# Optimization experiments

Measured on AMD Instinct MI355X. Metric: run time of the kernel, lower is better.

Reference implementation:

```python
import jax, jax.numpy as jnp
import numpy as np
from jax import lax

B, N, NC = 16, 25200, 80
CONF_THRES = 0.25
IOU_THRES = 0.45
TOP_K = 1024      # pre-NMS candidates (fixed for jit)
MAX_DET = 300     # max detections kept per image (YOLOv5 default)
MAX_WH = 4096.0   # per-class box offset trick (class-aware NMS)
IMG = 640.0


def setup_inputs() -> dict:
    key = jax.random.key(0)
    k1, k2 = jax.random.split(key)
    raw = jax.random.uniform(k1, (B, N, 5 + NC), dtype=jnp.float32)
    # xywh boxes in pixel coords, obj/cls scores in [0,1]
    xy = raw[..., :2] * IMG
    wh = raw[..., 2:4] * 128.0 + 4.0
    scores = raw[..., 4:]
    detections = jnp.concatenate([xy, wh, scores], axis=-1)
    return {"detections": detections}


def _xywh2xyxy(b):
    xy, wh = b[..., :2], b[..., 2:4]
    half = wh * 0.5
    return jnp.concatenate([xy - half, xy + half], axis=-1)


def _iou_matrix(b):  # b: [K,4] xyxy -> [K,K]
    area = jnp.maximum(b[:, 2] - b[:, 0], 0.0) * jnp.maximum(b[:, 3] - b[:, 1], 0.0)
    lt = jnp.maximum(b[:, None, :2], b[None, :, :2])
    rb = jnp.minimum(b[:, None, 2:], b[None, :, 2:])
    wh = jnp.maximum(rb - lt, 0.0)
    inter = wh[..., 0] * wh[..., 1]
    return inter / (area[:, None] + area[None, :] - inter + 1e-7)


def _nms_single(det):  # det: [N, 5+NC] -> [MAX_DET, 6] (x1,y1,x2,y2,conf,cls)
    obj = det[:, 4]
    cls_scores = det[:, 5:] * obj[:, None]          # conf = obj_conf * cls_conf
    conf = jnp.max(cls_scores, axis=-1)
    cls = jnp.argmax(cls_scores, axis=-1)
    valid = (obj > CONF_THRES) & (conf > CONF_THRES)
    conf = jnp.where(valid, conf, 0.0)
    boxes = _xywh2xyxy(det[:, :4])                  # [N,4]

    # top-K candidates by confidence (already sorted descending)
    scores_k, idx = lax.top_k(conf, TOP_K)
    boxes_k = boxes[idx]                            # [K,4]
    cls_k = cls[idx]
    # class-aware NMS via coordinate offset per class
    offs = cls_k.astype(boxes_k.dtype) * MAX_WH
    iou = _iou_matrix(boxes_k + offs[:, None])      # [K,K]

    # greedy suppression (candidates sorted by score descending)
    def body(i, keep):
        sup = (jnp.arange(TOP_K) > i) & keep[i] & (iou[i] > IOU_THRES)
        return keep & ~sup

    keep = lax.fori_loop(0, TOP_K, body, scores_k > 0.0)

    final_scores = jnp.where(keep, scores_k, 0.0)
    s, order = lax.top_k(final_scores, MAX_DET)
    out = jnp.concatenate(
        [boxes_k[order], s[:, None], cls_k[order].astype(boxes_k.dtype)[:, None]],
        axis=-1,
    )  # [MAX_DET, 6]
    return jnp.where(s[:, None] > 0.0, out, 0.0)


def reference(detections):
    return jax.vmap(_nms_single)(detections)  # [B, MAX_DET, 6]
```

## Files before the change

### kernel.cpp

```cpp
#include <hip/hip_runtime.h>
#include <stdint.h>

#define B_ 16
#define N_ 25200
#define NC_ 80
#define ROW_ 85
#define TOPK_ 1024
#define MAXDET_ 300
#define CONF_T 0.25f
#define IOU_T 0.45f
#define MAX_WH_ 4096.0f
#define NBINS_ 16384
#define CBUF_CAP 4096

typedef unsigned long long u64;
typedef unsigned int u32;

#define OFF_KEYS  0ull
#define OFF_T     0ull
#define OFF_OBOX  3225600ull
#define OFF_OAR   3487744ull
#define OFF_PAY   3553280ull
#define OFF_VALID 3946496ull

#define K1_ROWS 64
#define K1_TPB  ((N_ + K1_ROWS - 1) / K1_ROWS)
#define K1_TILES (K1_TPB * B_)
#define K1_GRID 768
#define K1_SLOTS 24
#define K1_BUF_F4 (K1_SLOTS * 64)

__device__ __forceinline__ void k1_stage(const float4* __restrict__ src4, int cnt4,
                                         float4* buf, int wid, int lane) {
#pragma unroll
    for (int k = 0; k < 6; ++k) {
        const int s = k * 4 + wid;
        const int f = s * 64 + lane;
        const float4* g = src4 + min(f, cnt4 - 1);
        float4* l = buf + s * 64;
        __builtin_amdgcn_global_load_lds(
            (const __attribute__((address_space(1))) void*)g,
            (__attribute__((address_space(3))) void*)l, 16, 0, 0);
    }
}

__global__ void __launch_bounds__(256) score_kernel(const float* __restrict__ det,
                                                    u64* __restrict__ keys) {
#pragma clang fp contract(off)
    __shared__ float4 sbuf[2 * K1_BUF_F4];
    const int t = threadIdx.x;
    const int wid = t >> 6;
    const int lane = t & 63;

    int tid = blockIdx.x;
    {
        const int b0 = tid / K1_TPB, tk0 = tid % K1_TPB;
        const int r00 = tk0 * K1_ROWS;
        const int rows0 = min(K1_ROWS, N_ - r00);
        const float4* src4 = (const float4*)(det + ((size_t)b0 * N_ + r00) * ROW_);
        k1_stage(src4, rows0 * ROW_ / 4, &sbuf[0], wid, lane);
    }
    int p = 0;
    while (tid < K1_TILES) {
        const int b = tid / K1_TPB, tk = tid % K1_TPB;
        const int r0 = tk * K1_ROWS;
        const int rows = min(K1_ROWS, N_ - r0);
        const int next = tid + K1_GRID;
        const bool has_next = (next < K1_TILES);
        if (has_next) {
            const int nb = next / K1_TPB, ntk = next % K1_TPB;
            const int nr0 = ntk * K1_ROWS;
            const int nrows = min(K1_ROWS, N_ - nr0);
            const float4* nsrc4 = (const float4*)(det + ((size_t)nb * N_ + nr0) * ROW_);
            k1_stage(nsrc4, nrows * ROW_ / 4, &sbuf[(1 - p) * K1_BUF_F4], wid, lane);
            asm volatile("s_waitcnt vmcnt(6)" ::: "memory");
        } else {
            asm volatile("s_waitcnt vmcnt(0)" ::: "memory");
        }
        __builtin_amdgcn_sched_barrier(0);
        __builtin_amdgcn_s_barrier();

        const float* sp = (const float*)&sbuf[p * K1_BUF_F4];
        const int row = t >> 2;
        const int h = t & 3;
        const bool rv = (row < rows);
        float m = -1.0f;
        float obj = 0.0f;
        if (rv) {
            const float* rp = sp + row * ROW_;
            obj = rp[4];
#pragma unroll
            for (int c = 0; c < 20; ++c) {
                float pr = obj * rp[5 + h * 20 + c];
                m = (pr > m) ? pr : m;
            }
        }
        m = fmaxf(m, __shfl_xor(m, 1));
        m = fmaxf(m, __shfl_xor(m, 2));
        float conf = (rv && obj > CONF_T && m > CONF_T) ? m : 0.0f;
        u64 key = ((u64)__float_as_uint(conf) << 32) |
                  (u32)(0xFFFFFFFFu - (u32)(r0 + row));
        if (rv && h == 0) keys[(size_t)b * N_ + r0 + row] = key;

        __builtin_amdgcn_s_barrier();
        p ^= 1;
        tid = next;
    }
}

__global__ void __launch_bounds__(1024) select_kernel(const u64* __restrict__ keys,
                                                      const float* __restrict__ det,
                                                      float4* __restrict__ obox4,
                                                      float* __restrict__ oar,
                                                      float* __restrict__ pay,
                                                      int* __restrict__ valid) {
#pragma clang fp contract(off)
    const int b = blockIdx.x;
    const int t = threadIdx.x;
    const int lane = t & 63;
    const int wid = t >> 6;
    __shared__ u32 hist16k[NBINS_];
    __shared__ u64 cbuf[CBUF_CAP];
    __shared__ u64 sorted[TOPK_];
    __shared__ u32 hist256[256];
    __shared__ u32 wtot[16];
    __shared__ u64 s_prefix;
    __shared__ int s_k, s_cnt, s_cutd, s_total;

    const u64* bkeys = keys + (size_t)b * N_;

    for (int i = t; i < NBINS_; i += 1024) hist16k[i] = 0;
    __syncthreads();
    for (int n = t; n < N_; n += 1024) {
        u64 key = bkeys[n];
        if ((key >> 32) != 0)
            atomicAdd(&hist16k[(u32)(key >> 44) & (NBINS_ - 1)], 1u);
    }
    __syncthreads();

    u32 h[16];
    u32 csum = 0;
#pragma unroll
    for (int q = 0; q < 16; ++q) { h[q] = hist16k[t * 16 + q]; csum += h[q]; }
    u32 suf = csum;
#pragma unroll
    for (int off = 1; off < 64; off <<= 1) {
        u32 v = __shfl_down(suf, off);
        if (lane + off < 64) suf += v;
    }
    if (lane == 0) wtot[wid] = suf;
    __syncthreads();
    if (t == 0) {
        u32 tot = 0;
        for (int w = 0; w < 16; ++w) tot += wtot[w];
        s_total = (int)tot;
        s_cutd = 0;
    }
    __syncthreads();
    u32 hi = 0;
    for (int w = wid + 1; w < 16; ++w) hi += wtot[w];
    u32 above = (suf - csum) + hi;
    u32 incl = above + csum;
    if (incl >= (u32)TOPK_ && above < (u32)TOPK_) {
        u32 cum = above;
        int cutd = t * 16;
        bool found = false;
#pragma unroll
        for (int q = 15; q >= 0; --q) {
            if (!found && cum + h[q] >= (u32)TOPK_) { cutd = t * 16 + q; found = true; }
            if (!found) cum += h[q];
        }
        s_cutd = cutd;
    }
    __syncthreads();
    const u32 cutd = (u32)s_cutd;
    const int total = s_total;

    if (t == 0) s_cnt = 0;
    __syncthreads();
    {
        int n = t;
        for (; n + 3 * 1024 < N_; n += 4096) {
            u64 k0 = bkeys[n];
            u64 k1 = bkeys[n + 1024];
            u64 k2 = bkeys[n + 2048];
            u64 k3 = bkeys[n + 3072];
            if ((k0 >> 32) != 0 && ((u32)(k0 >> 44) & (NBINS_ - 1)) >= cutd) { int p = atomicAdd(&s_cnt, 1); if (p < CBUF_CAP) cbuf[p] = k0; }
            if ((k1 >> 32) != 0 && ((u32)(k1 >> 44) & (NBINS_ - 1)) >= cutd) { int p = atomicAdd(&s_cnt, 1); if (p < CBUF_CAP) cbuf[p] = k1; }
            if ((k2 >> 32) != 0 && ((u32)(k2 >> 44) & (NBINS_ - 1)) >= cutd) { int p = atomicAdd(&s_cnt, 1); if (p < CBUF_CAP) cbuf[p] = k2; }
            if ((k3 >> 32) != 0 && ((u32)(k3 >> 44) & (NBINS_ - 1)) >= cutd) { int p = atomicAdd(&s_cnt, 1); if (p < CBUF_CAP) cbuf[p] = k3; }
        }
        for (; n < N_; n += 1024) {
            u64 key = bkeys[n];
            if ((key >> 32) != 0 && ((u32)(key >> 44) & (NBINS_ - 1)) >= cutd) { int p = atomicAdd(&s_cnt, 1); if (p < CBUF_CAP) cbuf[p] = key; }
        }
    }
    __syncthreads();
    const int cnt = min(s_cnt, CBUF_CAP);

    if (total >= TOPK_) {
        u64 prefix = 0;
        int k = TOPK_;
        for (int shift = 56; shift >= 0; shift -= 8) {
            if (t < 256) hist256[t] = 0;
            __syncthreads();
            for (int nn = t; nn < cnt; nn += 1024) {
                u64 key = cbuf[nn];
                if (shift == 56 || (key >> (shift + 8)) == prefix)
                    atomicAdd(&hist256[(u32)(key >> shift) & 255u], 1u);
            }
            __syncthreads();
            if (t < 64) {
                u32 b0 = hist256[t * 4 + 0], b1 = hist256[t * 4 + 1];
                u32 b2 = hist256[t * 4 + 2], b3 = hist256[t * 4 + 3];
                u32 sgrp = b0 + b1 + b2 + b3;
                u32 sufl = sgrp;
#pragma unroll
                for (int off = 1; off < 64; off <<= 1) {
                    u32 vv = __shfl(sufl, t + off);
                    sufl += (t + off < 64) ? vv : 0;
                }
                u32 A = sufl - sgrp;
                if (sufl >= (u32)k && A < (u32)k) {
                    u32 cum = A;
                    int d = t * 4;
                    bool found = false;
                    if (!found && cum + b3 >= (u32)k) { d = t * 4 + 3; found = true; }
                    if (!found) { cum += b3; if (cum + b2 >= (u32)k) { d = t * 4 + 2; found = true; } }
                    if (!found) { cum += b2; if (cum + b1 >= (u32)k) { d = t * 4 + 1; found = true; } }
                    if (!found) { cum += b1; if (cum + b0 >= (u32)k) { d = t * 4 + 0; found = true; } }
                    s_prefix = (prefix << 8) | (u64)d;
                    s_k = k - (int)cum;
                }
            }
            __syncthreads();
            prefix = s_prefix;
            k = s_k;
            __syncthreads();
        }
        const u64 T64 = prefix;

        if (t == 0) s_cnt = 0;
        __syncthreads();
        for (int nn = t; nn < cnt; nn += 1024) {
            u64 key = cbuf[nn];
            if (key >= T64) {
                int pos = atomicAdd(&s_cnt, 1);
                if (pos < TOPK_) sorted[pos] = key;
            }
        }
        __syncthreads();
    } else {
        for (int i = t; i < TOPK_; i += 1024)
            sorted[i] = (i < cnt) ? cbuf[i] : (u64)(u32)(0xFFFFFFFFu - (u32)i);
        __syncthreads();
    }

    for (int kk = 2; kk <= TOPK_; kk <<= 1) {
        for (int j = kk >> 1; j > 0; j >>= 1) {
            __syncthreads();
            int partner = t ^ j;
            if (partner > t) {
                u64 a = sorted[t], c = sorted[partner];
                bool desc = ((t & kk) == 0);
                if (desc ? (a < c) : (a > c)) { sorted[t] = c; sorted[partner] = a; }
            }
        }
    }
    __syncthreads();

    u64 myk = sorted[t];
    int n_idx = (int)(0xFFFFFFFFu - (u32)myk);
    float conf = __uint_as_float((u32)(myk >> 32));
    const float* row = det + ((size_t)b * N_ + n_idx) * ROW_;
    float xc = row[0], yc = row[1], w = row[2], hh2 = row[3];
    float obj = row[4];
    float m = -1.0f;
    int cls = 0;
    for (int c = 0; c < NC_; ++c) {
        float p = obj * row[5 + c];
        if (p > m) { m = p; cls = c; }
    }
    float hw = w * 0.5f, hh = hh2 * 0.5f;
    float x1 = xc - hw, y1 = yc - hh, x2 = xc + hw, y2 = yc + hh;
    float off = (float)cls * MAX_WH_;
    float X1 = x1 + off, Y1 = y1 + off, X2 = x2 + off, Y2 = y2 + off;
    float area = fmaxf(X2 - X1, 0.0f) * fmaxf(Y2 - Y1, 0.0f);

    size_t o = (size_t)b * TOPK_ + t;
    obox4[o] = make_float4(X1, Y1, X2, Y2);
    oar[o] = area;
    float* p6 = pay + o * 6;
    p6[0] = x1; p6[1] = y1; p6[2] = x2; p6[3] = y2;
    p6[4] = conf; p6[5] = (float)cls;
    valid[o] = (conf > 0.0f) ? 1 : 0;
}

__global__ void __launch_bounds__(256) mask_kernel(const float4* __restrict__ obox4,
                                                   const float* __restrict__ oar,
                                                   u64* __restrict__ T) {
#pragma clang fp contract(off)
    __shared__ float4 sbox[TOPK_];
    __shared__ float sar[TOPK_];
    const int b = blockIdx.y;
    const int t = threadIdx.x;
    for (int i = t; i < TOPK_; i += 256) {
        sbox[i] = obox4[(size_t)b * TOPK_ + i];
        sar[i] = oar[(size_t)b * TOPK_ + i];
    }
    __syncthreads();
    const int j = blockIdx.x * 16 + (t >> 4);
    const int w = t & 15;
    float4 bj = sbox[j];
    float aj = sar[j];
    u64 m = 0;
#pragma unroll 4
    for (int jj = 0; jj < 64; ++jj) {
        int r = (jj + 5 * w) & 63;
        int i = (w << 6) | r;
        float4 bi = sbox[i];
        float ai = sar[i];
        float lx = fmaxf(bi.x, bj.x);
        float ly = fmaxf(bi.y, bj.y);
        float rx = fminf(bi.z, bj.z);
        float ry = fminf(bi.w, bj.w);
        float iw = fmaxf(rx - lx, 0.0f);
        float ih = fmaxf(ry - ly, 0.0f);
        float inter = iw * ih;
        float uni = ai + aj - inter + 1e-7f;
        bool sup = (inter / uni > IOU_T) && (j > i);
        m |= sup ? (1ull << r) : 0ull;
    }
    T[((size_t)b * TOPK_ + j) * 16 + w] = m;
}

__global__ void __launch_bounds__(64) scan_kernel(const u64* __restrict__ T,
                                                  const int* __restrict__ valid,
                                                  const float* __restrict__ pay,
                                                  float* __restrict__ out) {
    const int b = blockIdx.x;
    const int lane = threadIdx.x;
    u64 kept[16];
    bool done = false;
    int total = 0;

#pragma unroll
    for (int sw = 0; sw < 16; ++sw) {
        if (done) { kept[sw] = 0; continue; }
        const u64* col = T + ((size_t)(b * TOPK_ + sw * 64 + lane)) * 16;
        u64 tc[16];
#pragma unroll
        for (int q = 0; q < 8; ++q) {
            ulonglong2 v = reinterpret_cast<const ulonglong2*>(col)[q];
            tc[2 * q] = v.x;
            tc[2 * q + 1] = v.y;
        }
        int vint = valid[b * TOPK_ + sw * 64 + lane];
        u64 vw = __ballot(vint != 0);
        u64 rem_in = 0;
#pragma unroll
        for (int s = 0; s < 16; ++s) {
            if (s < sw) rem_in |= __ballot((kept[s] & tc[s]) != 0);
        }
        u64 Td = tc[sw];
        u64 K = 0;
        u64 R = (~vw) | rem_in;
        u64 U = ~(K | R);
        int guard = 0;
        while (U && guard++ < 64) {
            u64 S = Td & (K | U);
            bool inU = ((U >> lane) & 1ull) != 0;
            u64 nK = __ballot(inU && (S == 0));
            u64 nR = __ballot(inU && ((S & K) != 0));
            K |= nK;
            R |= nR;
            U &= ~(nK | nR);
        }
        kept[sw] = K;
        total += __popcll(K);
        if (total >= MAXDET_) done = true;
    }

    int cum = 0;
#pragma unroll
    for (int w = 0; w < 16; ++w) {
        u64 aw = kept[w];
        bool bit = ((aw >> lane) & 1ull) != 0;
        int rank = cum + __popcll(aw & ((1ull << lane) - 1ull));
        if (bit && rank < MAXDET_) {
            const float* p6 = pay + ((size_t)(b * TOPK_ + w * 64 + lane)) * 6;
            float* o = out + ((size_t)(b * MAXDET_ + rank)) * 6;
            o[0] = p6[0]; o[1] = p6[1]; o[2] = p6[2];
            o[3] = p6[3]; o[4] = p6[4]; o[5] = p6[5];
        }
        cum += __popcll(aw);
    }
    int kept_n = cum < MAXDET_ ? cum : MAXDET_;
    for (int i = kept_n * 6 + lane; i < MAXDET_ * 6; i += 64)
        out[(size_t)b * MAXDET_ * 6 + i] = 0.0f;
}

extern "C" void kernel_launch(void* const* d_in, const int* in_sizes, int n_in,
                              void* d_out, int out_size, void* d_ws, size_t ws_size,
                              hipStream_t stream) {
    const float* det = (const float*)d_in[0];
    float* out = (float*)d_out;
    char* ws = (char*)d_ws;

    u64* keys = (u64*)(ws + OFF_KEYS);
    u64* T = (u64*)(ws + OFF_T);
    float4* obox4 = (float4*)(ws + OFF_OBOX);
    float* oar = (float*)(ws + OFF_OAR);
    float* pay = (float*)(ws + OFF_PAY);
    int* valid = (int*)(ws + OFF_VALID);

    score_kernel<<<K1_GRID, 256, 0, stream>>>(det, keys);
    select_kernel<<<B_, 1024, 0, stream>>>(keys, det, obox4, oar, pay, valid);
    dim3 g4(TOPK_ / 16, B_);
    mask_kernel<<<g4, 256, 0, stream>>>(obox4, oar, T);
    scan_kernel<<<B_, 64, 0, stream>>>(T, valid, pay, out);
}
```

Baseline: 99.26 us.

## Fuse four NMS kernels into one cooperative kernel with grid syncs

Replaces the four separate launches (score, select, mask, scan) with one cooperative kernel of 256 blocks × 1024 threads that uses grid.sync between phases and a shared-memory union so each phase reuses the same LDS. The scoring phase is retiled to 128 rows per tile with 8 threads per row, and the candidate buffer is halved to 2048 entries. The aim is to remove launch gaps and per-kernel tail latency. In exchange, the select and scan phases run on only 16 blocks while the rest sit idle at grid barriers, and grid syncs carry their own cost. The smaller candidate buffer also risks overflow when many keys tie at the cut bin.

```diff
diff --git a/kernel.cpp b/kernel.cpp
--- a/kernel.cpp
+++ b/kernel.cpp
@@ -1,5 +1,8 @@
 #include <hip/hip_runtime.h>
+#include <hip/hip_cooperative_groups.h>
 #include <stdint.h>
+
+namespace cg = cooperative_groups;
 
 #define B_ 16
 #define N_ 25200
@@ -11,7 +14,7 @@
 #define IOU_T 0.45f
 #define MAX_WH_ 4096.0f
 #define NBINS_ 16384
-#define CBUF_CAP 4096
+#define CBUF_CAP 2048
 
 typedef unsigned long long u64;
 typedef unsigned int u32;
@@ -23,18 +26,18 @@
 #define OFF_PAY   3553280ull
 #define OFF_VALID 3946496ull
 
-#define K1_ROWS 64
+#define K1_ROWS 128
 #define K1_TPB  ((N_ + K1_ROWS - 1) / K1_ROWS)
 #define K1_TILES (K1_TPB * B_)
-#define K1_GRID 768
-#define K1_SLOTS 24
+#define GRID_ 256
+#define K1_SLOTS 48
 #define K1_BUF_F4 (K1_SLOTS * 64)
 
 __device__ __forceinline__ void k1_stage(const float4* __restrict__ src4, int cnt4,
                                          float4* buf, int wid, int lane) {
 #pragma unroll
-    for (int k = 0; k < 6; ++k) {
-        const int s = k * 4 + wid;
+    for (int k = 0; k < 3; ++k) {
+        const int s = k * 16 + wid;
         const int f = s * 64 + lane;
         const float4* g = src4 + min(f, cnt4 - 1);
         float4* l = buf + s * 64;
@@ -44,360 +47,365 @@
     }
 }
 
-__global__ void __launch_bounds__(256) score_kernel(const float* __restrict__ det,
-                                                    u64* __restrict__ keys) {
+__global__ void __launch_bounds__(1024, 4)
+fused_kernel(const float* __restrict__ det,
+             u64* __restrict__ keys,
+             u64* __restrict__ T,
+             float4* __restrict__ obox4,
+             float* __restrict__ oar,
+             float* __restrict__ pay,
+             int* __restrict__ valid,
+             float* __restrict__ out) {
 #pragma clang fp contract(off)
-    __shared__ float4 sbuf[2 * K1_BUF_F4];
+    __shared__ union {
+        float4 sbuf[2 * K1_BUF_F4];
+        struct {
+            u32 hist[NBINS_];
+            u64 cbuf[CBUF_CAP];
+            u64 sorted[TOPK_];
+            u32 hist256[256];
+            u32 wtot[16];
+        } sel;
+        struct {
+            float4 sbox[TOPK_];
+            float sar[TOPK_];
+        } msk;
+    } S;
+    __shared__ u64 s_prefix;
+    __shared__ int s_k, s_cnt, s_cutd, s_total;
+
+    cg::grid_group grid = cg::this_grid();
     const int t = threadIdx.x;
     const int wid = t >> 6;
     const int lane = t & 63;
 
-    int tid = blockIdx.x;
     {
-        const int b0 = tid / K1_TPB, tk0 = tid % K1_TPB;
-        const int r00 = tk0 * K1_ROWS;
-        const int rows0 = min(K1_ROWS, N_ - r00);
-        const float4* src4 = (const float4*)(det + ((size_t)b0 * N_ + r00) * ROW_);
-        k1_stage(src4, rows0 * ROW_ / 4, &sbuf[0], wid, lane);
+        int tid = blockIdx.x;
+        if (tid < K1_TILES) {
+            {
+                const int b0 = tid / K1_TPB, tk0 = tid % K1_TPB;
+                const int r00 = tk0 * K1_ROWS;
+                const int rows0 = min(K1_ROWS, N_ - r00);
+                const float4* src4 = (const float4*)(det + ((size_t)b0 * N_ + r00) * ROW_);
+                k1_stage(src4, rows0 * ROW_ / 4, &S.sbuf[0], wid, lane);
+            }
+            int p = 0;
+            while (tid < K1_TILES) {
+                const int b = tid / K1_TPB, tk = tid % K1_TPB;
+                const int r0 = tk * K1_ROWS;
+                const int rows = min(K1_ROWS, N_ - r0);
+                const int next = tid + GRID_;
+                if (next < K1_TILES) {
+                    const int nb = next / K1_TPB, ntk = next % K1_TPB;
+                    const int nr0 = ntk * K1_ROWS;
+                    const int nrows = min(K1_ROWS, N_ - nr0);
+                    const float4* nsrc4 = (const float4*)(det + ((size_t)nb * N_ + nr0) * ROW_);
+                    k1_stage(nsrc4, nrows * ROW_ / 4, &S.sbuf[(1 - p) * K1_BUF_F4], wid, lane);
+                    asm volatile("s_waitcnt vmcnt(3)" ::: "memory");
+                } else {
+                    asm volatile("s_waitcnt vmcnt(0)" ::: "memory");
+                }
+                __builtin_amdgcn_sched_barrier(0);
+                __builtin_amdgcn_s_barrier();
+
+                const float* sp = (const float*)&S.sbuf[p * K1_BUF_F4];
+                const int row = t >> 3;
+                const int h = t & 7;
+                const bool rv = (row < rows);
+                float m = -1.0f;
+                float obj = 0.0f;
+                if (rv) {
+                    const float* rp = sp + row * ROW_;
+                    obj = rp[4];
+#pragma unroll
+                    for (int c = 0; c < 10; ++c) {
+                        float pr = obj * rp[5 + h * 10 + c];
+                        m = (pr > m) ? pr : m;
+                    }
+                }
+                m = fmaxf(m, __shfl_xor(m, 1));
+                m = fmaxf(m, __shfl_xor(m, 2));
+                m = fmaxf(m, __shfl_xor(m, 4));
+                float conf = (rv && obj > CONF_T && m > CONF_T) ? m : 0.0f;
+                u64 key = ((u64)__float_as_uint(conf) << 32) |
+                          (u32)(0xFFFFFFFFu - (u32)(r0 + row));
+                if (rv && h == 0) keys[(size_t)b * N_ + r0 + row] = key;
+
+                __builtin_amdgcn_s_barrier();
+                p ^= 1;
+                tid = next;
+            }
+        }
     }
-    int p = 0;
-    while (tid < K1_TILES) {
-        const int b = tid / K1_TPB, tk = tid % K1_TPB;
-        const int r0 = tk * K1_ROWS;
-        const int rows = min(K1_ROWS, N_ - r0);
-        const int next = tid + K1_GRID;
-        const bool has_next = (next < K1_TILES);
-        if (has_next) {
-            const int nb = next / K1_TPB, ntk = next % K1_TPB;
-            const int nr0 = ntk * K1_ROWS;
-            const int nrows = min(K1_ROWS, N_ - nr0);
-            const float4* nsrc4 = (const float4*)(det + ((size_t)nb * N_ + nr0) * ROW_);
-            k1_stage(nsrc4, nrows * ROW_ / 4, &sbuf[(1 - p) * K1_BUF_F4], wid, lane);
-            asm volatile("s_waitcnt vmcnt(6)" ::: "memory");
-        } else {
-            asm volatile("s_waitcnt vmcnt(0)" ::: "memory");
-        }
-        __builtin_amdgcn_sched_barrier(0);
-        __builtin_amdgcn_s_barrier();
-
-        const float* sp = (const float*)&sbuf[p * K1_BUF_F4];
-        const int row = t >> 2;
-        const int h = t & 3;
-        const bool rv = (row < rows);
-        float m = -1.0f;
-        float obj = 0.0f;
-        if (rv) {
-            const float* rp = sp + row * ROW_;
-            obj = rp[4];
-#pragma unroll
-            for (int c = 0; c < 20; ++c) {
-                float pr = obj * rp[5 + h * 20 + c];
-                m = (pr > m) ? pr : m;
-            }
-        }
-        m = fmaxf(m, __shfl_xor(m, 1));
-        m = fmaxf(m, __shfl_xor(m, 2));
-        float conf = (rv && obj > CONF_T && m > CONF_T) ? m : 0.0f;
-        u64 key = ((u64)__float_as_uint(conf) << 32) |
-                  (u32)(0xFFFFFFFFu - (u32)(r0 + row));
-        if (rv && h == 0) keys[(size_t)b * N_ + r0 + row] = key;
-
-        __builtin_amdgcn_s_barrier();
-        p ^= 1;
-        tid = next;
-    }
-}
-
-__global__ void __launch_bounds__(1024) select_kernel(const u64* __restrict__ keys,
-                                                      const float* __restrict__ det,
-                                                      float4* __restrict__ obox4,
-                                                      float* __restrict__ oar,
-                                                      float* __restrict__ pay,
-                                                      int* __restrict__ valid) {
-#pragma clang fp contract(off)
-    const int b = blockIdx.x;
-    const int t = threadIdx.x;
-    const int lane = t & 63;
-    const int wid = t >> 6;
-    __shared__ u32 hist16k[NBINS_];
-    __shared__ u64 cbuf[CBUF_CAP];
-    __shared__ u64 sorted[TOPK_];
-    __shared__ u32 hist256[256];
-    __shared__ u32 wtot[16];
-    __shared__ u64 s_prefix;
-    __shared__ int s_k, s_cnt, s_cutd, s_total;
-
-    const u64* bkeys = keys + (size_t)b * N_;
-
-    for (int i = t; i < NBINS_; i += 1024) hist16k[i] = 0;
-    __syncthreads();
-    for (int n = t; n < N_; n += 1024) {
-        u64 key = bkeys[n];
-        if ((key >> 32) != 0)
-            atomicAdd(&hist16k[(u32)(key >> 44) & (NBINS_ - 1)], 1u);
-    }
-    __syncthreads();
-
-    u32 h[16];
-    u32 csum = 0;
-#pragma unroll
-    for (int q = 0; q < 16; ++q) { h[q] = hist16k[t * 16 + q]; csum += h[q]; }
-    u32 suf = csum;
-#pragma unroll
-    for (int off = 1; off < 64; off <<= 1) {
-        u32 v = __shfl_down(suf, off);
-        if (lane + off < 64) suf += v;
-    }
-    if (lane == 0) wtot[wid] = suf;
-    __syncthreads();
-    if (t == 0) {
-        u32 tot = 0;
-        for (int w = 0; w < 16; ++w) tot += wtot[w];
-        s_total = (int)tot;
-        s_cutd = 0;
-    }
-    __syncthreads();
-    u32 hi = 0;
-    for (int w = wid + 1; w < 16; ++w) hi += wtot[w];
-    u32 above = (suf - csum) + hi;
-    u32 incl = above + csum;
-    if (incl >= (u32)TOPK_ && above < (u32)TOPK_) {
-        u32 cum = above;
-        int cutd = t * 16;
-        bool found = false;
-#pragma unroll
-        for (int q = 15; q >= 0; --q) {
-            if (!found && cum + h[q] >= (u32)TOPK_) { cutd = t * 16 + q; found = true; }
-            if (!found) cum += h[q];
-        }
-        s_cutd = cutd;
-    }
-    __syncthreads();
-    const u32 cutd = (u32)s_cutd;
-    const int total = s_total;
-
-    if (t == 0) s_cnt = 0;
-    __syncthreads();
-    {
-        int n = t;
-        for (; n + 3 * 1024 < N_; n += 4096) {
-            u64 k0 = bkeys[n];
-            u64 k1 = bkeys[n + 1024];
-            u64 k2 = bkeys[n + 2048];
-            u64 k3 = bkeys[n + 3072];
-            if ((k0 >> 32) != 0 && ((u32)(k0 >> 44) & (NBINS_ - 1)) >= cutd) { int p = atomicAdd(&s_cnt, 1); if (p < CBUF_CAP) cbuf[p] = k0; }
-            if ((k1 >> 32) != 0 && ((u32)(k1 >> 44) & (NBINS_ - 1)) >= cutd) { int p = atomicAdd(&s_cnt, 1); if (p < CBUF_CAP) cbuf[p] = k1; }
-            if ((k2 >> 32) != 0 && ((u32)(k2 >> 44) & (NBINS_ - 1)) >= cutd) { int p = atomicAdd(&s_cnt, 1); if (p < CBUF_CAP) cbuf[p] = k2; }
-            if ((k3 >> 32) != 0 && ((u32)(k3 >> 44) & (NBINS_ - 1)) >= cutd) { int p = atomicAdd(&s_cnt, 1); if (p < CBUF_CAP) cbuf[p] = k3; }
-        }
-        for (; n < N_; n += 1024) {
+    grid.sync();
+
+    if (blockIdx.x < B_) {
+        const int b = blockIdx.x;
+        const u64* bkeys = keys + (size_t)b * N_;
+
+        for (int i = t; i < NBINS_; i += 1024) S.sel.hist[i] = 0;
+        __syncthreads();
+        for (int n = t; n < N_; n += 1024) {
             u64 key = bkeys[n];
-            if ((key >> 32) != 0 && ((u32)(key >> 44) & (NBINS_ - 1)) >= cutd) { int p = atomicAdd(&s_cnt, 1); if (p < CBUF_CAP) cbuf[p] = key; }
-        }
-    }
-    __syncthreads();
-    const int cnt = min(s_cnt, CBUF_CAP);
-
-    if (total >= TOPK_) {
-        u64 prefix = 0;
-        int k = TOPK_;
-        for (int shift = 56; shift >= 0; shift -= 8) {
-            if (t < 256) hist256[t] = 0;
+            if ((key >> 32) != 0)
+                atomicAdd(&S.sel.hist[(u32)(key >> 44) & (NBINS_ - 1)], 1u);
+        }
+        __syncthreads();
+
+        u32 h[16];
+        u32 csum = 0;
+#pragma unroll
+        for (int q = 0; q < 16; ++q) { h[q] = S.sel.hist[t * 16 + q]; csum += h[q]; }
+        u32 suf = csum;
+#pragma unroll
+        for (int off = 1; off < 64; off <<= 1) {
+            u32 v = __shfl_down(suf, off);
+            if (lane + off < 64) suf += v;
+        }
+        if (lane == 0) S.sel.wtot[wid] = suf;
+        __syncthreads();
+        if (t == 0) {
+            u32 tot = 0;
+            for (int w = 0; w < 16; ++w) tot += S.sel.wtot[w];
+            s_total = (int)tot;
+            s_cutd = 0;
+        }
+        __syncthreads();
+        u32 hi = 0;
+        for (int w = wid + 1; w < 16; ++w) hi += S.sel.wtot[w];
+        u32 above = (suf - csum) + hi;
+        u32 incl = above + csum;
+        if (incl >= (u32)TOPK_ && above < (u32)TOPK_) {
+            u32 cum = above;
+            int cutd = t * 16;
+            bool found = false;
+#pragma unroll
+            for (int q = 15; q >= 0; --q) {
+                if (!found && cum + h[q] >= (u32)TOPK_) { cutd = t * 16 + q; found = true; }
+                if (!found) cum += h[q];
+            }
+            s_cutd = cutd;
+        }
+        __syncthreads();
+        const u32 cutd = (u32)s_cutd;
+        const int total = s_total;
+
+        if (t == 0) s_cnt = 0;
+        __syncthreads();
+        {
+            int n = t;
+            for (; n + 3 * 1024 < N_; n += 4096) {
+                u64 k0 = bkeys[n];
+                u64 k1 = bkeys[n + 1024];
+                u64 k2 = bkeys[n + 2048];
+                u64 k3 = bkeys[n + 3072];
+                if ((k0 >> 32) != 0 && ((u32)(k0 >> 44) & (NBINS_ - 1)) >= cutd) { int p = atomicAdd(&s_cnt, 1); if (p < CBUF_CAP) S.sel.cbuf[p] = k0; }
+                if ((k1 >> 32) != 0 && ((u32)(k1 >> 44) & (NBINS_ - 1)) >= cutd) { int p = atomicAdd(&s_cnt, 1); if (p < CBUF_CAP) S.sel.cbuf[p] = k1; }
+                if ((k2 >> 32) != 0 && ((u32)(k2 >> 44) & (NBINS_ - 1)) >= cutd) { int p = atomicAdd(&s_cnt, 1); if (p < CBUF_CAP) S.sel.cbuf[p] = k2; }
+                if ((k3 >> 32) != 0 && ((u32)(k3 >> 44) & (NBINS_ - 1)) >= cutd) { int p = atomicAdd(&s_cnt, 1); if (p < CBUF_CAP) S.sel.cbuf[p] = k3; }
+            }
+            for (; n < N_; n += 1024) {
+                u64 key = bkeys[n];
+                if ((key >> 32) != 0 && ((u32)(key >> 44) & (NBINS_ - 1)) >= cutd) { int p = atomicAdd(&s_cnt, 1); if (p < CBUF_CAP) S.sel.cbuf[p] = key; }
+            }
+        }
+        __syncthreads();
+        const int cnt = min(s_cnt, CBUF_CAP);
+
+        if (total >= TOPK_) {
+            u64 prefix = 0;
+            int k = TOPK_;
+            for (int shift = 56; shift >= 0; shift -= 8) {
+                if (t < 256) S.sel.hist256[t] = 0;
+                __syncthreads();
+                for (int nn = t; nn < cnt; nn += 1024) {
+                    u64 key = S.sel.cbuf[nn];
+                    if (shift == 56 || (key >> (shift + 8)) == prefix)
+                        atomicAdd(&S.sel.hist256[(u32)(key >> shift) & 255u], 1u);
+                }
+                __syncthreads();
+                if (t < 64) {
+                    u32 b0 = S.sel.hist256[t * 4 + 0], b1 = S.sel.hist256[t * 4 + 1];
+                    u32 b2 = S.sel.hist256[t * 4 + 2], b3 = S.sel.hist256[t * 4 + 3];
+                    u32 sgrp = b0 + b1 + b2 + b3;
+                    u32 sufl = sgrp;
+#pragma unroll
+                    for (int off = 1; off < 64; off <<= 1) {
+                        u32 vv = __shfl(sufl, t + off);
+                        sufl += (t + off < 64) ? vv : 0;
+                    }
+                    u32 A = sufl - sgrp;
+                    if (sufl >= (u32)k && A < (u32)k) {
+                        u32 cum = A;
+                        int d = t * 4;
+                        bool found = false;
+                        if (!found && cum + b3 >= (u32)k) { d = t * 4 + 3; found = true; }
+                        if (!found) { cum += b3; if (cum + b2 >= (u32)k) { d = t * 4 + 2; found = true; } }
+                        if (!found) { cum += b2; if (cum + b1 >= (u32)k) { d = t * 4 + 1; found = true; } }
+                        if (!found) { cum += b1; if (cum + b0 >= (u32)k) { d = t * 4 + 0; found = true; } }
+                        s_prefix = (prefix << 8) | (u64)d;
+                        s_k = k - (int)cum;
+                    }
+                }
+                __syncthreads();
+                prefix = s_prefix;
+                k = s_k;
+                __syncthreads();
+            }
+            const u64 T64 = prefix;
+
+            if (t == 0) s_cnt = 0;
             __syncthreads();
             for (int nn = t; nn < cnt; nn += 1024) {
-                u64 key = cbuf[nn];
-                if (shift == 56 || (key >> (shift + 8)) == prefix)
-                    atomicAdd(&hist256[(u32)(key >> shift) & 255u], 1u);
+                u64 key = S.sel.cbuf[nn];
+                if (key >= T64) {
+                    int pos = atomicAdd(&s_cnt, 1);
+                    if (pos < TOPK_) S.sel.sorted[pos] = key;
+                }
             }
             __syncthreads();
-            if (t < 64) {
-                u32 b0 = hist256[t * 4 + 0], b1 = hist256[t * 4 + 1];
-                u32 b2 = hist256[t * 4 + 2], b3 = hist256[t * 4 + 3];
-                u32 sgrp = b0 + b1 + b2 + b3;
-                u32 sufl = sgrp;
-#pragma unroll
-                for (int off = 1; off < 64; off <<= 1) {
-                    u32 vv = __shfl(sufl, t + off);
-                    sufl += (t + off < 64) ? vv : 0;
-                }
-                u32 A = sufl - sgrp;
-                if (sufl >= (u32)k && A < (u32)k) {
-                    u32 cum = A;
-                    int d = t * 4;
-                    bool found = false;
-                    if (!found && cum + b3 >= (u32)k) { d = t * 4 + 3; found = true; }
-                    if (!found) { cum += b3; if (cum + b2 >= (u32)k) { d = t * 4 + 2; found = true; } }
-                    if (!found) { cum += b2; if (cum + b1 >= (u32)k) { d = t * 4 + 1; found = true; } }
-                    if (!found) { cum += b1; if (cum + b0 >= (u32)k) { d = t * 4 + 0; found = true; } }
-                    s_prefix = (prefix << 8) | (u64)d;
-                    s_k = k - (int)cum;
-                }
-            }
+        } else {
+            for (int i = t; i < TOPK_; i += 1024)
+                S.sel.sorted[i] = (i < cnt) ? S.sel.cbuf[i]
+                                            : (u64)(u32)(0xFFFFFFFFu - (u32)i);
             __syncthreads();
-            prefix = s_prefix;
-            k = s_k;
-            __syncthreads();
-        }
-        const u64 T64 = prefix;
-
-        if (t == 0) s_cnt = 0;
-        __syncthreads();
-        for (int nn = t; nn < cnt; nn += 1024) {
-            u64 key = cbuf[nn];
-            if (key >= T64) {
-                int pos = atomicAdd(&s_cnt, 1);
-                if (pos < TOPK_) sorted[pos] = key;
-            }
-        }
-        __syncthreads();
-    } else {
-        for (int i = t; i < TOPK_; i += 1024)
-            sorted[i] = (i < cnt) ? cbuf[i] : (u64)(u32)(0xFFFFFFFFu - (u32)i);
-        __syncthreads();
+        }
+
+        for (int kk = 2; kk <= TOPK_; kk <<= 1) {
+            for (int j = kk >> 1; j > 0; j >>= 1) {
+                __syncthreads();
+                int partner = t ^ j;
+                if (partner > t) {
+                    u64 a = S.sel.sorted[t], c = S.sel.sorted[partner];
+                    bool desc = ((t & kk) == 0);
+                    if (desc ? (a < c) : (a > c)) { S.sel.sorted[t] = c; S.sel.sorted[partner] = a; }
+                }
+            }
+        }
+        __syncthreads();
+
+        u64 myk = S.sel.sorted[t];
+        int n_idx = (int)(0xFFFFFFFFu - (u32)myk);
+        float conf = __uint_as_float((u32)(myk >> 32));
+        const float* row = det + ((size_t)b * N_ + n_idx) * ROW_;
+        float xc = row[0], yc = row[1], w = row[2], hh2 = row[3];
+        float obj = row[4];
+        float m = -1.0f;
+        int cls = 0;
+        for (int c = 0; c < NC_; ++c) {
+            float p = obj * row[5 + c];
+            if (p > m) { m = p; cls = c; }
+        }
+        float hw = w * 0.5f, hh = hh2 * 0.5f;
+        float x1 = xc - hw, y1 = yc - hh, x2 = xc + hw, y2 = yc + hh;
+        float off = (float)cls * MAX_WH_;
+        float X1 = x1 + off, Y1 = y1 + off, X2 = x2 + off, Y2 = y2 + off;
+        float area = fmaxf(X2 - X1, 0.0f) * fmaxf(Y2 - Y1, 0.0f);
+
+        size_t o = (size_t)b * TOPK_ + t;
+        obox4[o] = make_float4(X1, Y1, X2, Y2);
+        oar[o] = area;
+        float* p6 = pay + o * 6;
+        p6[0] = x1; p6[1] = y1; p6[2] = x2; p6[3] = y2;
+        p6[4] = conf; p6[5] = (float)cls;
+        valid[o] = (conf > 0.0f) ? 1 : 0;
     }
-
-    for (int kk = 2; kk <= TOPK_; kk <<= 1) {
-        for (int j = kk >> 1; j > 0; j >>= 1) {
-            __syncthreads();
-            int partner = t ^ j;
-            if (partner > t) {
-                u64 a = sorted[t], c = sorted[partner];
-                bool desc = ((t & kk) == 0);
-                if (desc ? (a < c) : (a > c)) { sorted[t] = c; sorted[partner] = a; }
-            }
-        }
+    grid.sync();
+
+    {
+        const int u = blockIdx.x;
+        const int b = u >> 4;
+        const int cg_ = u & 15;
+        S.msk.sbox[t] = obox4[(size_t)b * TOPK_ + t];
+        S.msk.sar[t] = oar[(size_t)b * TOPK_ + t];
+        __syncthreads();
+        const int j = cg_ * 64 + (t >> 4);
+        const int w = t & 15;
+        float4 bj = S.msk.sbox[j];
+        float aj = S.msk.sar[j];
+        u64 m = 0;
+#pragma unroll 4
+        for (int jj = 0; jj < 64; ++jj) {
+            int r = (jj + 5 * w) & 63;
+            int i = (w << 6) | r;
+            float4 bi = S.msk.sbox[i];
+            float ai = S.msk.sar[i];
+            float lx = fmaxf(bi.x, bj.x);
+            float ly = fmaxf(bi.y, bj.y);
+            float rx = fminf(bi.z, bj.z);
+            float ry = fminf(bi.w, bj.w);
+            float iw = fmaxf(rx - lx, 0.0f);
+            float ih = fmaxf(ry - ly, 0.0f);
+            float inter = iw * ih;
+            float uni = ai + aj - inter + 1e-7f;
+            bool sup = (inter / uni > IOU_T) && (j > i);
+            m |= sup ? (1ull << r) : 0ull;
+        }
+        T[((size_t)b * TOPK_ + j) * 16 + w] = m;
     }
-    __syncthreads();
-
-    u64 myk = sorted[t];
-    int n_idx = (int)(0xFFFFFFFFu - (u32)myk);
-    float conf = __uint_as_float((u32)(myk >> 32));
-    const float* row = det + ((size_t)b * N_ + n_idx) * ROW_;
-    float xc = row[0], yc = row[1], w = row[2], hh2 = row[3];
-    float obj = row[4];
-    float m = -1.0f;
-    int cls = 0;
-    for (int c = 0; c < NC_; ++c) {
-        float p = obj * row[5 + c];
-        if (p > m) { m = p; cls = c; }
+    grid.sync();
+
+    if (blockIdx.x < B_ && t < 64) {
+        const int b = blockIdx.x;
+        u64 kept[16];
+        bool done = false;
+        int total = 0;
+
+#pragma unroll
+        for (int sw = 0; sw < 16; ++sw) {
+            if (done) { kept[sw] = 0; continue; }
+            const u64* col = T + ((size_t)(b * TOPK_ + sw * 64 + lane)) * 16;
+            u64 tc[16];
+#pragma unroll
+            for (int q = 0; q < 8; ++q) {
+                ulonglong2 v = reinterpret_cast<const ulonglong2*>(col)[q];
+                tc[2 * q] = v.x;
+                tc[2 * q + 1] = v.y;
+            }
+            int vint = valid[b * TOPK_ + sw * 64 + lane];
+            u64 vw = __ballot(vint != 0);
+            u64 rem_in = 0;
+#pragma unroll
+            for (int s = 0; s < 16; ++s) {
+                if (s < sw) rem_in |= __ballot((kept[s] & tc[s]) != 0);
+            }
+            u64 Td = tc[sw];
+            u64 K = 0;
+            u64 R = (~vw) | rem_in;
+            u64 U = ~(K | R);
+            int guard = 0;
+            while (U && guard++ < 64) {
+                u64 Sx = Td & (K | U);
+                bool inU = ((U >> lane) & 1ull) != 0;
+                u64 nK = __ballot(inU && (Sx == 0));
+                u64 nR = __ballot(inU && ((Sx & K) != 0));
+                K |= nK;
+                R |= nR;
+                U &= ~(nK | nR);
+            }
+            kept[sw] = K;
+            total += __popcll(K);
+            if (total >= MAXDET_) done = true;
+        }
+
+        int cum = 0;
+#pragma unroll
+        for (int w = 0; w < 16; ++w) {
+            u64 aw = kept[w];
+            bool bit = ((aw >> lane) & 1ull) != 0;
+            int rank = cum + __popcll(aw & ((1ull << lane) - 1ull));
+            if (bit && rank < MAXDET_) {
+                const float* p6 = pay + ((size_t)(b * TOPK_ + w * 64 + lane)) * 6;
+                float* o = out + ((size_t)(b * MAXDET_ + rank)) * 6;
+                o[0] = p6[0]; o[1] = p6[1]; o[2] = p6[2];
+                o[3] = p6[3]; o[4] = p6[4]; o[5] = p6[5];
+            }
+            cum += __popcll(aw);
+        }
+        int kept_n = cum < MAXDET_ ? cum : MAXDET_;
+        for (int i = kept_n * 6 + lane; i < MAXDET_ * 6; i += 64)
+            out[(size_t)b * MAXDET_ * 6 + i] = 0.0f;
     }
-    float hw = w * 0.5f, hh = hh2 * 0.5f;
-    float x1 = xc - hw, y1 = yc - hh, x2 = xc + hw, y2 = yc + hh;
-    float off = (float)cls * MAX_WH_;
-    float X1 = x1 + off, Y1 = y1 + off, X2 = x2 + off, Y2 = y2 + off;
-    float area = fmaxf(X2 - X1, 0.0f) * fmaxf(Y2 - Y1, 0.0f);
-
-    size_t o = (size_t)b * TOPK_ + t;
-    obox4[o] = make_float4(X1, Y1, X2, Y2);
-    oar[o] = area;
-    float* p6 = pay + o * 6;
-    p6[0] = x1; p6[1] = y1; p6[2] = x2; p6[3] = y2;
-    p6[4] = conf; p6[5] = (float)cls;
-    valid[o] = (conf > 0.0f) ? 1 : 0;
-}
-
-__global__ void __launch_bounds__(256) mask_kernel(const float4* __restrict__ obox4,
-                                                   const float* __restrict__ oar,
-                                                   u64* __restrict__ T) {
-#pragma clang fp contract(off)
-    __shared__ float4 sbox[TOPK_];
-    __shared__ float sar[TOPK_];
-    const int b = blockIdx.y;
-    const int t = threadIdx.x;
-    for (int i = t; i < TOPK_; i += 256) {
-        sbox[i] = obox4[(size_t)b * TOPK_ + i];
-        sar[i] = oar[(size_t)b * TOPK_ + i];
-    }
-    __syncthreads();
-    const int j = blockIdx.x * 16 + (t >> 4);
-    const int w = t & 15;
-    float4 bj = sbox[j];
-    float aj = sar[j];
-    u64 m = 0;
-#pragma unroll 4
-    for (int jj = 0; jj < 64; ++jj) {
-        int r = (jj + 5 * w) & 63;
-        int i = (w << 6) | r;
-        float4 bi = sbox[i];
-        float ai = sar[i];
-        float lx = fmaxf(bi.x, bj.x);
-        float ly = fmaxf(bi.y, bj.y);
-        float rx = fminf(bi.z, bj.z);
-        float ry = fminf(bi.w, bj.w);
-        float iw = fmaxf(rx - lx, 0.0f);
-        float ih = fmaxf(ry - ly, 0.0f);
-        float inter = iw * ih;
-        float uni = ai + aj - inter + 1e-7f;
-        bool sup = (inter / uni > IOU_T) && (j > i);
-        m |= sup ? (1ull << r) : 0ull;
-    }
-    T[((size_t)b * TOPK_ + j) * 16 + w] = m;
-}
-
-__global__ void __launch_bounds__(64) scan_kernel(const u64* __restrict__ T,
-                                                  const int* __restrict__ valid,
-                                                  const float* __restrict__ pay,
-                                                  float* __restrict__ out) {
-    const int b = blockIdx.x;
-    const int lane = threadIdx.x;
-    u64 kept[16];
-    bool done = false;
-    int total = 0;
-
-#pragma unroll
-    for (int sw = 0; sw < 16; ++sw) {
-        if (done) { kept[sw] = 0; continue; }
-        const u64* col = T + ((size_t)(b * TOPK_ + sw * 64 + lane)) * 16;
-        u64 tc[16];
-#pragma unroll
-        for (int q = 0; q < 8; ++q) {
-            ulonglong2 v = reinterpret_cast<const ulonglong2*>(col)[q];
-            tc[2 * q] = v.x;
-            tc[2 * q + 1] = v.y;
-        }
-        int vint = valid[b * TOPK_ + sw * 64 + lane];
-        u64 vw = __ballot(vint != 0);
-        u64 rem_in = 0;
-#pragma unroll
-        for (int s = 0; s < 16; ++s) {
-            if (s < sw) rem_in |= __ballot((kept[s] & tc[s]) != 0);
-        }
-        u64 Td = tc[sw];
-        u64 K = 0;
-        u64 R = (~vw) | rem_in;
-        u64 U = ~(K | R);
-        int guard = 0;
-        while (U && guard++ < 64) {
-            u64 S = Td & (K | U);
-            bool inU = ((U >> lane) & 1ull) != 0;
-            u64 nK = __ballot(inU && (S == 0));
-            u64 nR = __ballot(inU && ((S & K) != 0));
-            K |= nK;
-            R |= nR;
-            U &= ~(nK | nR);
-        }
-        kept[sw] = K;
-        total += __popcll(K);
-        if (total >= MAXDET_) done = true;
-    }
-
-    int cum = 0;
-#pragma unroll
-    for (int w = 0; w < 16; ++w) {
-        u64 aw = kept[w];
-        bool bit = ((aw >> lane) & 1ull) != 0;
-        int rank = cum + __popcll(aw & ((1ull << lane) - 1ull));
-        if (bit && rank < MAXDET_) {
-            const float* p6 = pay + ((size_t)(b * TOPK_ + w * 64 + lane)) * 6;
-            float* o = out + ((size_t)(b * MAXDET_ + rank)) * 6;
-            o[0] = p6[0]; o[1] = p6[1]; o[2] = p6[2];
-            o[3] = p6[3]; o[4] = p6[4]; o[5] = p6[5];
-        }
-        cum += __popcll(aw);
-    }
-    int kept_n = cum < MAXDET_ ? cum : MAXDET_;
-    for (int i = kept_n * 6 + lane; i < MAXDET_ * 6; i += 64)
-        out[(size_t)b * MAXDET_ * 6 + i] = 0.0f;
 }
 
 extern "C" void kernel_launch(void* const* d_in, const int* in_sizes, int n_in,
@@ -414,9 +422,8 @@
     float* pay = (float*)(ws + OFF_PAY);
     int* valid = (int*)(ws + OFF_VALID);
 
-    score_kernel<<<K1_GRID, 256, 0, stream>>>(det, keys);
-    select_kernel<<<B_, 1024, 0, stream>>>(keys, det, obox4, oar, pay, valid);
-    dim3 g4(TOPK_ / 16, B_);
-    mask_kernel<<<g4, 256, 0, stream>>>(obox4, oar, T);
-    scan_kernel<<<B_, 64, 0, stream>>>(T, valid, pay, out);
+    void* args[] = {(void*)&det, (void*)&keys, (void*)&T, (void*)&obox4,
+                    (void*)&oar, (void*)&pay, (void*)&valid, (void*)&out};
+    hipLaunchCooperativeKernel((void*)fused_kernel, dim3(GRID_), dim3(1024),
+                               args, 0, stream);
 }
```

New measurement: 194.8 us. 96.3% more time.

## Fuse NMS scan into mask kernel via last-block atomic ticket

Applied to the files above, without the earlier changes.

Merges the suppression-mask kernel and the greedy scan kernel into one launch. Each image's 64 mask blocks bump a per-image atomic counter, and the block that draws the last ticket runs the scan for that image. The counter is reset inside the select kernel. This removes one kernel launch and its inter-kernel gap, at the cost of fences and an atomic in every mask block, and the scan now runs on the tail of whichever block finishes last.

```diff
diff --git a/kernel.cpp b/kernel.cpp
--- a/kernel.cpp
+++ b/kernel.cpp
@@ -22,6 +22,7 @@
 #define OFF_OAR   3487744ull
 #define OFF_PAY   3553280ull
 #define OFF_VALID 3946496ull
+#define OFF_DONE  4012032ull
 
 #define K1_ROWS 64
 #define K1_TPB  ((N_ + K1_ROWS - 1) / K1_ROWS)
@@ -66,8 +67,7 @@
         const int r0 = tk * K1_ROWS;
         const int rows = min(K1_ROWS, N_ - r0);
         const int next = tid + K1_GRID;
-        const bool has_next = (next < K1_TILES);
-        if (has_next) {
+        if (next < K1_TILES) {
             const int nb = next / K1_TPB, ntk = next % K1_TPB;
             const int nr0 = ntk * K1_ROWS;
             const int nrows = min(K1_ROWS, N_ - nr0);
@@ -113,7 +113,8 @@
                                                       float4* __restrict__ obox4,
                                                       float* __restrict__ oar,
                                                       float* __restrict__ pay,
-                                                      int* __restrict__ valid) {
+                                                      int* __restrict__ valid,
+                                                      int* __restrict__ done) {
 #pragma clang fp contract(off)
     const int b = blockIdx.x;
     const int t = threadIdx.x;
@@ -126,6 +127,8 @@
     __shared__ u32 wtot[16];
     __shared__ u64 s_prefix;
     __shared__ int s_k, s_cnt, s_cutd, s_total;
+
+    if (t == 0) done[b] = 0;
 
     const u64* bkeys = keys + (size_t)b * N_;
 
@@ -296,12 +299,17 @@
     valid[o] = (conf > 0.0f) ? 1 : 0;
 }
 
-__global__ void __launch_bounds__(256) mask_kernel(const float4* __restrict__ obox4,
-                                                   const float* __restrict__ oar,
-                                                   u64* __restrict__ T) {
+__global__ void __launch_bounds__(256) mask_scan_kernel(const float4* __restrict__ obox4,
+                                                        const float* __restrict__ oar,
+                                                        u64* __restrict__ T,
+                                                        const int* __restrict__ valid,
+                                                        const float* __restrict__ pay,
+                                                        float* __restrict__ out,
+                                                        int* __restrict__ done) {
 #pragma clang fp contract(off)
     __shared__ float4 sbox[TOPK_];
     __shared__ float sar[TOPK_];
+    __shared__ int s_ticket;
     const int b = blockIdx.y;
     const int t = threadIdx.x;
     for (int i = t; i < TOPK_; i += 256) {
@@ -332,21 +340,25 @@
         m |= sup ? (1ull << r) : 0ull;
     }
     T[((size_t)b * TOPK_ + j) * 16 + w] = m;
-}
-
-__global__ void __launch_bounds__(64) scan_kernel(const u64* __restrict__ T,
-                                                  const int* __restrict__ valid,
-                                                  const float* __restrict__ pay,
-                                                  float* __restrict__ out) {
-    const int b = blockIdx.x;
-    const int lane = threadIdx.x;
+
+    __syncthreads();
+    if (t == 0) {
+        __threadfence();
+        s_ticket = __hip_atomic_fetch_add(&done[b], 1, __ATOMIC_ACQ_REL,
+                                          __HIP_MEMORY_SCOPE_AGENT);
+        __threadfence();
+    }
+    __syncthreads();
+    if (s_ticket != 63 || t >= 64) return;
+
+    const int lane = t;
     u64 kept[16];
-    bool done = false;
+    bool donef = false;
     int total = 0;
 
 #pragma unroll
     for (int sw = 0; sw < 16; ++sw) {
-        if (done) { kept[sw] = 0; continue; }
+        if (donef) { kept[sw] = 0; continue; }
         const u64* col = T + ((size_t)(b * TOPK_ + sw * 64 + lane)) * 16;
         u64 tc[16];
 #pragma unroll
@@ -368,27 +380,27 @@
         u64 U = ~(K | R);
         int guard = 0;
         while (U && guard++ < 64) {
-            u64 S = Td & (K | U);
+            u64 Sx = Td & (K | U);
             bool inU = ((U >> lane) & 1ull) != 0;
-            u64 nK = __ballot(inU && (S == 0));
-            u64 nR = __ballot(inU && ((S & K) != 0));
+            u64 nK = __ballot(inU && (Sx == 0));
+            u64 nR = __ballot(inU && ((Sx & K) != 0));
             K |= nK;
             R |= nR;
             U &= ~(nK | nR);
         }
         kept[sw] = K;
         total += __popcll(K);
-        if (total >= MAXDET_) done = true;
+        if (total >= MAXDET_) donef = true;
     }
 
     int cum = 0;
 #pragma unroll
-    for (int w = 0; w < 16; ++w) {
-        u64 aw = kept[w];
+    for (int w2 = 0; w2 < 16; ++w2) {
+        u64 aw = kept[w2];
         bool bit = ((aw >> lane) & 1ull) != 0;
         int rank = cum + __popcll(aw & ((1ull << lane) - 1ull));
         if (bit && rank < MAXDET_) {
-            const float* p6 = pay + ((size_t)(b * TOPK_ + w * 64 + lane)) * 6;
+            const float* p6 = pay + ((size_t)(b * TOPK_ + w2 * 64 + lane)) * 6;
             float* o = out + ((size_t)(b * MAXDET_ + rank)) * 6;
             o[0] = p6[0]; o[1] = p6[1]; o[2] = p6[2];
             o[3] = p6[3]; o[4] = p6[4]; o[5] = p6[5];
@@ -413,10 +425,10 @@
     float* oar = (float*)(ws + OFF_OAR);
     float* pay = (float*)(ws + OFF_PAY);
     int* valid = (int*)(ws + OFF_VALID);
+    int* done = (int*)(ws + OFF_DONE);
 
     score_kernel<<<K1_GRID, 256, 0, stream>>>(det, keys);
-    select_kernel<<<B_, 1024, 0, stream>>>(keys, det, obox4, oar, pay, valid);
-    dim3 g4(TOPK_ / 16, B_);
-    mask_kernel<<<g4, 256, 0, stream>>>(obox4, oar, T);
-    scan_kernel<<<B_, 64, 0, stream>>>(T, valid, pay, out);
+    select_kernel<<<B_, 1024, 0, stream>>>(keys, det, obox4, oar, pay, valid, done);
+    dim3 g3(TOPK_ / 16, B_);
+    mask_scan_kernel<<<g3, 256, 0, stream>>>(obox4, oar, T, valid, pay, out, done);
 }
```

New measurement: 145.6 us. 1.47x slower.
